# Kernel tuning notes

Measured on AMD Instinct MI355X. Metric: run time of the kernel, lower is better.

## Reference

```python
import jax, jax.numpy as jnp
import numpy as np

# Config constants (match init_kwargs / config)
B = 16        # config.BATCH_SIZE
T = 2048      # config.TRAIN_LEN
C = 256       # input channels (input_shape[-1])
K = 8         # kernel_size
F = 256       # nb_filters
DIL = 4       # dilation_rate


def setup_inputs() -> dict:
    key = jax.random.key(0)
    k1, k2, k3 = jax.random.split(key, 3)
    inputs = jax.random.normal(k1, (B, T, C), dtype=jnp.float32)
    kernel = jax.random.normal(k2, (C, K, F), dtype=jnp.float32) * 0.05
    bias = jax.random.normal(k3, (F,), dtype=jnp.float32) * 0.05
    return {"inputs": inputs, "kernel": kernel, "bias": bias}


def reference(inputs, kernel, bias):
    # Original TF layer computes, per (b,t,k,f):
    #   raw[b,t,k,f] = sum_c (x[b,t,c] * kernel[c,k,f] + bias[f])
    #               = conv[b,t,k,f] + C * bias[f]
    # (bias is added BEFORE the reduce_sum over the channel axis, so it is
    #  scaled by C — we reproduce that quirk faithfully.)
    # Then each (t,k) slice is scatter-added to output time t + k*dilation
    # (the gather_nd + zero-pad construction in TF implements exactly this
    #  dilated transposed-conv scatter; non-matching positions gather zeros),
    # and finally the last T timesteps are kept.
    Bq, Tq, Cq = inputs.shape
    Kq, Fq = kernel.shape[1], kernel.shape[2]
    conv = jnp.einsum('btc,ckf->btkf', inputs, kernel) + jnp.asarray(Cq, inputs.dtype) * bias
    L = Tq + (Kq - 1) * DIL  # final_time_len
    # scatter positions: out[i + j*DIL] += conv[:, i, j, :]
    pos = (jnp.arange(Tq)[:, None] + DIL * jnp.arange(Kq)[None, :]).reshape(-1)  # (T*K,)
    out = jnp.zeros((Bq, L, Fq), dtype=conv.dtype)
    out = out.at[:, pos, :].add(conv.reshape(Bq, Tq * Kq, Fq))
    return out[:, -Tq:, :]
```

## Files before the change

### kernel.cpp

```cpp
#include <hip/hip_runtime.h>
#include <hip/hip_bf16.h>


#define B_    16
#define T_    2048
#define C_    256
#define KT    8
#define F_    256
#define DILL  4
#define SH    28
#define BT    64
#define ROWS  (BT + SH)

typedef __attribute__((ext_vector_type(8))) short short8;
typedef __attribute__((ext_vector_type(4))) float floatx4;

__global__ __launch_bounds__(256) void wprep_kernel(const float* __restrict__ W,
                                                    ushort* __restrict__ Wf) {
    const int o    = blockIdx.x * 256 + threadIdx.x;
    const int i    = o & 7;
    const int lane = (o >> 3) & 63;
    const int g    = (o >> 9) & 15;
    const int cs   = (o >> 13) & 7;
    const int j    = o >> 16;
    const int c    = cs * 32 + (lane >> 4) * 8 + i;
    const int f    = g * 16 + (lane & 15);
    __hip_bfloat16 h = __float2bfloat16(W[(c * KT + j) * F_ + f]);
    Wf[o] = *reinterpret_cast<const ushort*>(&h);
}

__global__ __launch_bounds__(256, 2) void deconv_kernel(
        const float* __restrict__ x, const ushort* __restrict__ Wf,
        const float* __restrict__ bias, float* __restrict__ out) {
    __shared__ ushort xs[ROWS * C_];
    const int t0  = blockIdx.x * BT;
    const int b   = blockIdx.y;
    const int tid = threadIdx.x;

    for (int idx = tid; idx < ROWS * 32; idx += 256) {
        const int row = idx >> 5, cb = idx & 31;
        const int t = t0 + row;
        float v[8] = {0.f,0.f,0.f,0.f,0.f,0.f,0.f,0.f};
        if (t < T_) {
            const float4* p = reinterpret_cast<const float4*>(
                x + ((b * T_ + t) * C_ + cb * 8));
            float4 u0 = p[0], u1 = p[1];
            v[0]=u0.x; v[1]=u0.y; v[2]=u0.z; v[3]=u0.w;
            v[4]=u1.x; v[5]=u1.y; v[6]=u1.z; v[7]=u1.w;
        }
        short8 pk;
        #pragma unroll
        for (int i = 0; i < 8; ++i) {
            __hip_bfloat16 h = __float2bfloat16(v[i]);
            pk[i] = *reinterpret_cast<const short*>(&h);
        }
        const int sc = cb ^ (row & 7);
        *reinterpret_cast<short8*>(&xs[row * C_ + sc * 8]) = pk;
    }

    const int lane = tid & 63, wave = tid >> 6;
    const int l16 = lane & 15, q = lane >> 4;

    float bf4[4];
    #pragma unroll
    for (int nf = 0; nf < 4; ++nf) bf4[nf] = bias[(wave * 4 + nf) * 16 + l16];

    __syncthreads();

    floatx4 acc[4][4];
    #pragma unroll
    for (int mf = 0; mf < 4; ++mf)
        #pragma unroll
        for (int nf = 0; nf < 4; ++nf)
            acc[mf][nf] = (floatx4){0.f, 0.f, 0.f, 0.f};

    const ushort* wbase = Wf + wave * 2048 + lane * 8;

#define LOAD_A(s_, arr) do {                                              \
        const int j_ = (s_) >> 3, cs_ = (s_) & 7;                         \
        const int shift_ = SH - 4 * j_;                                   \
        _Pragma("unroll")                                                 \
        for (int mf = 0; mf < 4; ++mf) {                                  \
            const int row_ = mf * 16 + l16 + shift_;                      \
            const int ch_  = ((cs_ << 2) + q) ^ (row_ & 7);               \
            arr[mf] = *reinterpret_cast<const short8*>(                   \
                &xs[row_ * C_ + ch_ * 8]);                                \
        } } while (0)

#define LOAD_B(s_, arr) do {                                              \
        const ushort* p_ = wbase + (s_) * 8192;                           \
        _Pragma("unroll")                                                 \
        for (int nf = 0; nf < 4; ++nf)                                    \
            arr[nf] = *reinterpret_cast<const short8*>(p_ + nf * 512);    \
        } while (0)

#define DO_MFMA(aa, bb) do {                                              \
        _Pragma("unroll")                                                 \
        for (int mf = 0; mf < 4; ++mf)                                    \
            _Pragma("unroll")                                             \
            for (int nf = 0; nf < 4; ++nf)                                \
                acc[mf][nf] = __builtin_amdgcn_mfma_f32_16x16x32_bf16(    \
                    aa[mf], bb[nf], acc[mf][nf], 0, 0, 0);                \
        } while (0)

    short8 a0[4], b0[4], a1[4], b1[4];
    LOAD_A(0, a0); LOAD_B(0, b0);
    LOAD_A(1, a1); LOAD_B(1, b1);

    for (int s = 0; s < 64; s += 2) {
        DO_MFMA(a0, b0);
        const int sp2 = (s + 2) & 63;
        LOAD_A(sp2, a0); LOAD_B(sp2, b0);
        DO_MFMA(a1, b1);
        const int sp3 = (s + 3) & 63;
        LOAD_A(sp3, a1); LOAD_B(sp3, b1);
    }

    #pragma unroll
    for (int nf = 0; nf < 4; ++nf) {
        const int f = (wave * 4 + nf) * 16 + l16;
        #pragma unroll
        for (int mf = 0; mf < 4; ++mf) {
            #pragma unroll
            for (int r = 0; r < 4; ++r) {
                const int t = t0 + mf * 16 + q * 4 + r;
                const int jmin = (t < T_ - SH) ? 0 : (((t - (T_ - SH)) >> 2) + 1);
                out[(b * T_ + t) * F_ + f] =
                    acc[mf][nf][r] + (float)(8 - jmin) * 256.0f * bf4[nf];
            }
        }
    }
#undef LOAD_A
#undef LOAD_B
#undef DO_MFMA
}

extern "C" void kernel_launch(void* const* d_in, const int* in_sizes, int n_in,
                              void* d_out, int out_size, void* d_ws, size_t ws_size,
                              hipStream_t stream) {
    const float* x    = (const float*)d_in[0];
    const float* W    = (const float*)d_in[1];
    const float* bias = (const float*)d_in[2];
    float* out = (float*)d_out;
    ushort* Wf = (ushort*)d_ws;

    wprep_kernel<<<(KT * F_ * C_) / 256, 256, 0, stream>>>(W, Wf);
    dim3 grid(T_ / BT, B_);
    deconv_kernel<<<grid, 256, 0, stream>>>(x, Wf, bias, out);
}
```

Baseline: 48.04 us.

## Double time tile to 128 rows with 8 waves and vectorize weight prep

The main kernel now covers 128 timesteps per block with 512 threads (8 waves). Each wave computes an 8x2 MFMA fragment grid instead of 4x4, which raises reuse of the shared-memory input tile relative to the 28-row halo and halves the block count. The weight-prep kernel now has each thread write one packed 8-element bf16 vector instead of a single scalar. In exchange, shared memory per block grows, each wave holds more A fragments in registers, and the smaller grid (256 blocks) may leave some compute units underused.

```diff
diff --git a/kernel.cpp b/kernel.cpp
--- a/kernel.cpp
+++ b/kernel.cpp
@@ -9,7 +9,7 @@
 #define F_    256
 #define DILL  4
 #define SH    28
-#define BT    64
+#define BT    128
 #define ROWS  (BT + SH)
 
 typedef __attribute__((ext_vector_type(8))) short short8;
@@ -17,19 +17,24 @@
 
 __global__ __launch_bounds__(256) void wprep_kernel(const float* __restrict__ W,
                                                     ushort* __restrict__ Wf) {
-    const int o    = blockIdx.x * 256 + threadIdx.x;
-    const int i    = o & 7;
-    const int lane = (o >> 3) & 63;
-    const int g    = (o >> 9) & 15;
-    const int cs   = (o >> 13) & 7;
-    const int j    = o >> 16;
-    const int c    = cs * 32 + (lane >> 4) * 8 + i;
+    const int tid  = threadIdx.x;
+    const int fid  = blockIdx.x * 4 + (tid >> 6);
+    const int lane = tid & 63;
+    const int g    = fid & 15;
+    const int cs   = (fid >> 4) & 7;
+    const int j    = fid >> 7;
+    const int c0   = cs * 32 + (lane >> 4) * 8;
     const int f    = g * 16 + (lane & 15);
-    __hip_bfloat16 h = __float2bfloat16(W[(c * KT + j) * F_ + f]);
-    Wf[o] = *reinterpret_cast<const ushort*>(&h);
+    short8 pk;
+    #pragma unroll
+    for (int i = 0; i < 8; ++i) {
+        __hip_bfloat16 h = __float2bfloat16(W[((c0 + i) * KT + j) * F_ + f]);
+        pk[i] = *reinterpret_cast<const short*>(&h);
+    }
+    *reinterpret_cast<short8*>(Wf + fid * 512 + lane * 8) = pk;
 }
 
-__global__ __launch_bounds__(256, 2) void deconv_kernel(
+__global__ __launch_bounds__(512, 2) void deconv_kernel(
         const float* __restrict__ x, const ushort* __restrict__ Wf,
         const float* __restrict__ bias, float* __restrict__ out) {
     __shared__ ushort xs[ROWS * C_];
@@ -37,7 +42,7 @@
     const int b   = blockIdx.y;
     const int tid = threadIdx.x;
 
-    for (int idx = tid; idx < ROWS * 32; idx += 256) {
+    for (int idx = tid; idx < ROWS * 32; idx += 512) {
         const int row = idx >> 5, cb = idx & 31;
         const int t = t0 + row;
         float v[8] = {0.f,0.f,0.f,0.f,0.f,0.f,0.f,0.f};
@@ -61,26 +66,26 @@
     const int lane = tid & 63, wave = tid >> 6;
     const int l16 = lane & 15, q = lane >> 4;
 
-    float bf4[4];
+    float bf2[2];
     #pragma unroll
-    for (int nf = 0; nf < 4; ++nf) bf4[nf] = bias[(wave * 4 + nf) * 16 + l16];
+    for (int nf = 0; nf < 2; ++nf) bf2[nf] = bias[wave * 32 + nf * 16 + l16];
 
     __syncthreads();
 
-    floatx4 acc[4][4];
+    floatx4 acc[8][2];
     #pragma unroll
-    for (int mf = 0; mf < 4; ++mf)
+    for (int mf = 0; mf < 8; ++mf)
         #pragma unroll
-        for (int nf = 0; nf < 4; ++nf)
+        for (int nf = 0; nf < 2; ++nf)
             acc[mf][nf] = (floatx4){0.f, 0.f, 0.f, 0.f};
 
-    const ushort* wbase = Wf + wave * 2048 + lane * 8;
+    const ushort* wbase = Wf + wave * 1024 + lane * 8;
 
 #define LOAD_A(s_, arr) do {                                              \
         const int j_ = (s_) >> 3, cs_ = (s_) & 7;                         \
         const int shift_ = SH - 4 * j_;                                   \
         _Pragma("unroll")                                                 \
-        for (int mf = 0; mf < 4; ++mf) {                                  \
+        for (int mf = 0; mf < 8; ++mf) {                                  \
             const int row_ = mf * 16 + l16 + shift_;                      \
             const int ch_  = ((cs_ << 2) + q) ^ (row_ & 7);               \
             arr[mf] = *reinterpret_cast<const short8*>(                   \
@@ -90,20 +95,20 @@
 #define LOAD_B(s_, arr) do {                                              \
         const ushort* p_ = wbase + (s_) * 8192;                           \
         _Pragma("unroll")                                                 \
-        for (int nf = 0; nf < 4; ++nf)                                    \
+        for (int nf = 0; nf < 2; ++nf)                                    \
             arr[nf] = *reinterpret_cast<const short8*>(p_ + nf * 512);    \
         } while (0)
 
 #define DO_MFMA(aa, bb) do {                                              \
         _Pragma("unroll")                                                 \
-        for (int mf = 0; mf < 4; ++mf)                                    \
+        for (int mf = 0; mf < 8; ++mf)                                    \
             _Pragma("unroll")                                             \
-            for (int nf = 0; nf < 4; ++nf)                                \
+            for (int nf = 0; nf < 2; ++nf)                                \
                 acc[mf][nf] = __builtin_amdgcn_mfma_f32_16x16x32_bf16(    \
                     aa[mf], bb[nf], acc[mf][nf], 0, 0, 0);                \
         } while (0)
 
-    short8 a0[4], b0[4], a1[4], b1[4];
+    short8 a0[8], b0[2], a1[8], b1[2];
     LOAD_A(0, a0); LOAD_B(0, b0);
     LOAD_A(1, a1); LOAD_B(1, b1);
 
@@ -117,16 +122,16 @@
     }
 
     #pragma unroll
-    for (int nf = 0; nf < 4; ++nf) {
-        const int f = (wave * 4 + nf) * 16 + l16;
+    for (int nf = 0; nf < 2; ++nf) {
+        const int f = wave * 32 + nf * 16 + l16;
         #pragma unroll
-        for (int mf = 0; mf < 4; ++mf) {
+        for (int mf = 0; mf < 8; ++mf) {
             #pragma unroll
             for (int r = 0; r < 4; ++r) {
                 const int t = t0 + mf * 16 + q * 4 + r;
                 const int jmin = (t < T_ - SH) ? 0 : (((t - (T_ - SH)) >> 2) + 1);
                 out[(b * T_ + t) * F_ + f] =
-                    acc[mf][nf][r] + (float)(8 - jmin) * 256.0f * bf4[nf];
+                    acc[mf][nf][r] + (float)(8 - jmin) * 256.0f * bf2[nf];
             }
         }
     }
@@ -144,7 +149,7 @@
     float* out = (float*)d_out;
     ushort* Wf = (ushort*)d_ws;
 
-    wprep_kernel<<<(KT * F_ * C_) / 256, 256, 0, stream>>>(W, Wf);
+    wprep_kernel<<<256, 256, 0, stream>>>(W, Wf);
     dim3 grid(T_ / BT, B_);
-    deconv_kernel<<<grid, 256, 0, stream>>>(x, Wf, bias, out);
+    deconv_kernel<<<grid, 512, 0, stream>>>(x, Wf, bias, out);
 }
```

After: 49.51 us. 3.1% more time.
